# Kernel optimization log

Hardware: AMD Instinct MI355X
Metric: run time of the kernel (lower is better)

The kernel has to match this reference:

```python
import jax, jax.numpy as jnp
import numpy as np

B, T, D, H, E, TOP_K = 2, 2048, 1024, 4096, 8, 2


def setup_inputs() -> dict:
    key = jax.random.key(0)
    ks = jax.random.split(key, 7)
    s_d = 1.0 / np.sqrt(D)
    s_h = 1.0 / np.sqrt(H)
    return {
        "x": jax.random.normal(ks[0], (B, T, D), dtype=jnp.float32),
        "gate_w": jax.random.uniform(ks[1], (D, E), minval=-s_d, maxval=s_d, dtype=jnp.float32),
        "gate_b": jax.random.uniform(ks[2], (E,), minval=-s_d, maxval=s_d, dtype=jnp.float32),
        "w1": jax.random.uniform(ks[3], (E, D, H), minval=-s_d, maxval=s_d, dtype=jnp.float32),
        "b1": jax.random.uniform(ks[4], (E, H), minval=-s_d, maxval=s_d, dtype=jnp.float32),
        "w2": jax.random.uniform(ks[5], (E, H, D), minval=-s_h, maxval=s_h, dtype=jnp.float32),
        "b2": jax.random.uniform(ks[6], (E, D), minval=-s_h, maxval=s_h, dtype=jnp.float32),
    }


def reference(x, gate_w, gate_b, w1, b1, w2, b2):
    Bsz, Tn, Din = x.shape
    x_flat = x.reshape(-1, Din)                       # [N, D]
    N = x_flat.shape[0]
    gating_logits = x_flat @ gate_w + gate_b          # [N, E]
    weights, indices = jax.lax.top_k(gating_logits, TOP_K)
    weights = jax.nn.softmax(weights, axis=-1).astype(x.dtype)
    # scatter top-k weights into dense dispatch tensor [N, E]
    dispatch = jnp.zeros((N, E), dtype=x.dtype).at[jnp.arange(N)[:, None], indices].set(weights)
    # NOTE: faithful to original - gate weight multiplies the expert INPUT
    # and again the expert OUTPUT (double weighting through the GELU MLP).
    dispatched_x = dispatch[:, :, None] * x_flat[:, None, :]       # [N, E, D]
    h = jax.nn.gelu(jnp.einsum('ned,edh->neh', dispatched_x, w1) + b1, approximate=False)
    expert_out = jnp.einsum('neh,ehd->ned', h, w2) + b2            # [N, E, D]
    combined = jnp.sum(dispatch[:, :, None] * expert_out, axis=1)  # [N, D]
    final = combined.reshape(Bsz, Tn, -1)
    return final, gating_logits
```

## Files before the change

kernel.cpp:

```cpp
#include <hip/hip_runtime.h>
#include <hip/hip_bf16.h>
#include <math.h>

#define NTOK 4096
#define DDIM 1024
#define HDIM 4096
#define NEXP 8
#define CAP  4096
#define ROWCAP 9216
#define MAXTILES 72

typedef __attribute__((ext_vector_type(8))) short short8;
typedef __attribute__((ext_vector_type(4))) float f32x4;

#define GLOAD_LDS16(g, l) __builtin_amdgcn_global_load_lds( \
    (const __attribute__((address_space(1))) void*)(g),     \
    (__attribute__((address_space(3))) void*)(l), 16, 0, 0)

__global__ __launch_bounds__(256) void gating_kernel(
    const float* __restrict__ x, const float* __restrict__ gw,
    const float* __restrict__ gb, float* __restrict__ logits_out,
    int* __restrict__ counts, int* __restrict__ tok, float* __restrict__ gate,
    int* __restrict__ eA, int* __restrict__ sA, float* __restrict__ gA) {
  int t = blockIdx.x;
  int tid = threadIdx.x;
  float p[NEXP];
#pragma unroll
  for (int e = 0; e < NEXP; ++e) p[e] = 0.f;
  const float* xr = x + (size_t)t * DDIM;
  for (int d = tid; d < DDIM; d += 256) {
    float xv = xr[d];
    const float* wr = gw + (size_t)d * NEXP;
#pragma unroll
    for (int e = 0; e < NEXP; ++e) p[e] += xv * wr[e];
  }
#pragma unroll
  for (int off = 32; off > 0; off >>= 1)
#pragma unroll
    for (int e = 0; e < NEXP; ++e) p[e] += __shfl_xor(p[e], off, 64);
  __shared__ float red[4][NEXP];
  int wave = tid >> 6, lane = tid & 63;
  if (lane == 0)
#pragma unroll
    for (int e = 0; e < NEXP; ++e) red[wave][e] = p[e];
  __syncthreads();
  if (tid < NEXP) {
    float v = red[0][tid] + red[1][tid] + red[2][tid] + red[3][tid] + gb[tid];
    logits_out[(size_t)t * NEXP + tid] = v;
    red[0][tid] = v;
  }
  __syncthreads();
  if (tid == 0) {
    float v[NEXP];
#pragma unroll
    for (int e = 0; e < NEXP; ++e) v[e] = red[0][e];
    int i0 = 0;
#pragma unroll
    for (int e = 1; e < NEXP; ++e) if (v[e] > v[i0]) i0 = e;
    int i1 = (i0 == 0) ? 1 : 0;
#pragma unroll
    for (int e = 0; e < NEXP; ++e) if (e != i0 && v[e] > v[i1]) i1 = e;
    float e1 = expf(v[i1] - v[i0]);
    float s = 1.f + e1;
    float g0 = 1.f / s, g1 = e1 / s;
    int s0 = atomicAdd(&counts[i0], 1);
    tok[i0 * CAP + s0] = t; gate[i0 * CAP + s0] = g0;
    int s1 = atomicAdd(&counts[i1], 1);
    tok[i1 * CAP + s1] = t; gate[i1 * CAP + s1] = g1;
    eA[2 * t] = i0; sA[2 * t] = s0; gA[2 * t] = g0;
    eA[2 * t + 1] = i1; sA[2 * t + 1] = s1; gA[2 * t + 1] = g1;
  }
}

__global__ void sched_kernel(const int* __restrict__ counts, int* __restrict__ poff,
                             int* __restrict__ tileE, int* __restrict__ tileR,
                             int* __restrict__ nTiles) {
  if (threadIdx.x == 0) {
    int acc = 0, nt = 0;
    for (int e = 0; e < NEXP; ++e) {
      poff[e] = acc;
      int tl = (counts[e] + 127) >> 7;
      for (int t = 0; t < tl; ++t) { tileE[nt] = e; tileR[nt] = acc + t * 128; ++nt; }
      acc += tl << 7;
    }
    poff[NEXP] = acc;
    nTiles[0] = nt;
  }
}

__global__ __launch_bounds__(256) void transpose_kernel(
    const float* __restrict__ in, __hip_bfloat16* __restrict__ out, int R, int C) {
  __shared__ float tile[64 * 65];
  int e = blockIdx.z;
  int c0 = blockIdx.x * 64, r0 = blockIdx.y * 64;
  const float* inp = in + (size_t)e * R * C;
  __hip_bfloat16* outp = out + (size_t)e * R * C;
  int tx = threadIdx.x & 15, ty = threadIdx.x >> 4;
#pragma unroll
  for (int i = 0; i < 64; i += 16) {
    float4 v = *(const float4*)(inp + (size_t)(r0 + ty + i) * C + c0 + tx * 4);
    float* dst = tile + (ty + i) * 65 + tx * 4;
    dst[0] = v.x; dst[1] = v.y; dst[2] = v.z; dst[3] = v.w;
  }
  __syncthreads();
  int c = threadIdx.x >> 3;
  int rb = (threadIdx.x & 7) * 8;
#pragma unroll
  for (int p = 0; p < 2; ++p) {
    int cc = c + p * 32;
    union { unsigned short u[8]; short8 v8; } pk;
#pragma unroll
    for (int j = 0; j < 8; ++j) {
      __hip_bfloat16 h = __float2bfloat16(tile[(rb + j) * 65 + cc]);
      pk.u[j] = *(unsigned short*)&h;
    }
    *(short8*)(outp + (size_t)(c0 + cc) * R + r0 + rb) = pk.v8;
  }
}

__global__ __launch_bounds__(256) void gather_kernel(
    const float* __restrict__ x, const int* __restrict__ counts,
    const int* __restrict__ poff, const int* __restrict__ tok,
    const float* __restrict__ gate, __hip_bfloat16* __restrict__ Xg) {
  int e = blockIdx.y, r = blockIdx.x;
  int pc = poff[e + 1] - poff[e];
  if (r >= pc) return;
  int row = poff[e] + r;
  int tid = threadIdx.x;
  __hip_bfloat16* orow = Xg + (size_t)row * DDIM;
  if (r < counts[e]) {
    int t = tok[e * CAP + r];
    float g = gate[e * CAP + r];
    float4 v = ((const float4*)(x + (size_t)t * DDIM))[tid];
    union { unsigned short u[4]; uint2 q; } pk;
    __hip_bfloat16 h0 = __float2bfloat16(v.x * g);
    __hip_bfloat16 h1 = __float2bfloat16(v.y * g);
    __hip_bfloat16 h2 = __float2bfloat16(v.z * g);
    __hip_bfloat16 h3 = __float2bfloat16(v.w * g);
    pk.u[0] = *(unsigned short*)&h0; pk.u[1] = *(unsigned short*)&h1;
    pk.u[2] = *(unsigned short*)&h2; pk.u[3] = *(unsigned short*)&h3;
    ((uint2*)orow)[tid] = pk.q;
  } else {
    uint2 z; z.x = 0; z.y = 0;
    ((uint2*)orow)[tid] = z;
  }
}

template <int EPI>
__global__ __launch_bounds__(256) void moe_gemm(
    const __hip_bfloat16* __restrict__ A, const __hip_bfloat16* __restrict__ B,
    const float* __restrict__ bias, __hip_bfloat16* __restrict__ Hout,
    float* __restrict__ Pout, const int* __restrict__ tileE,
    const int* __restrict__ tileR, const int* __restrict__ nTiles,
    int K, int Nn) {
  int ty = blockIdx.y;
  if (ty >= nTiles[0]) return;
  int e = tileE[ty];
  int rowBase = tileR[ty];
  int colBase = blockIdx.x * 128;

  __shared__ __align__(16) char As[128 * 64];
  __shared__ __align__(16) char Bs[128 * 64];

  const char* Ae = (const char*)A + (size_t)rowBase * K * 2;
  const char* Be = (const char*)B + ((size_t)e * Nn + colBase) * (size_t)K * 2;

  int tid = threadIdx.x;
  int wave = tid >> 6, lane = tid & 63;
  int srow = lane >> 2;
  int cg = (((lane & 3) ^ ((lane >> 3) & 3)) << 4);

  f32x4 acc[4][4] = {};

  int wm = (wave >> 1) * 64, wn = (wave & 1) * 64;
  int frm = lane & 15;
  int fsw = (((lane >> 4) ^ ((lane >> 1) & 3)) << 4);

  int kPer = (EPI == 1) ? (K >> 1) : K;
  int kLo = blockIdx.z * kPer, kHi = kLo + kPer;

  for (int k0 = kLo; k0 < kHi; k0 += 32) {
    __syncthreads();
#pragma unroll
    for (int c = 0; c < 2; ++c) {
      int ch = wave * 2 + c;
      int r = ch * 16 + srow;
      GLOAD_LDS16(Ae + ((size_t)r * K + k0) * 2 + cg, As + ch * 1024 + lane * 16);
      GLOAD_LDS16(Be + ((size_t)r * K + k0) * 2 + cg, Bs + ch * 1024 + lane * 16);
    }
    __syncthreads();
    short8 af[4], bfr[4];
#pragma unroll
    for (int i = 0; i < 4; ++i) {
      af[i]  = *(const short8*)(As + (wm + i * 16 + frm) * 64 + fsw);
      bfr[i] = *(const short8*)(Bs + (wn + i * 16 + frm) * 64 + fsw);
    }
#pragma unroll
    for (int i = 0; i < 4; ++i)
#pragma unroll
      for (int j = 0; j < 4; ++j)
        acc[i][j] = __builtin_amdgcn_mfma_f32_16x16x32_bf16(af[i], bfr[j], acc[i][j], 0, 0, 0);
  }

  int cq = lane >> 4, cn = lane & 15;
  if (EPI == 0) {
#pragma unroll
    for (int i = 0; i < 4; ++i) {
#pragma unroll
      for (int j = 0; j < 4; ++j) {
        int col = colBase + wn + j * 16 + cn;
        float bv = bias[e * Nn + col];
#pragma unroll
        for (int r = 0; r < 4; ++r) {
          int row = rowBase + wm + i * 16 + cq * 4 + r;
          float v = acc[i][j][r] + bv;
          v = 0.5f * v * (1.0f + erff(v * 0.70710678118f));
          Hout[(size_t)row * Nn + col] = __float2bfloat16(v);
        }
      }
    }
  } else {
    float* Pp = Pout + ((size_t)blockIdx.z * ROWCAP + rowBase) * DDIM;
#pragma unroll
    for (int i = 0; i < 4; ++i) {
#pragma unroll
      for (int j = 0; j < 4; ++j) {
        int col = colBase + wn + j * 16 + cn;
#pragma unroll
        for (int r = 0; r < 4; ++r) {
          int row = wm + i * 16 + cq * 4 + r;
          Pp[(size_t)row * DDIM + col] = acc[i][j][r];
        }
      }
    }
  }
}

__global__ __launch_bounds__(256) void combine_kernel(
    const float* __restrict__ P, const float* __restrict__ b2,
    const int* __restrict__ poff, const int* __restrict__ eA,
    const int* __restrict__ sA, const float* __restrict__ gA,
    float* __restrict__ outF) {
  int t = blockIdx.x, c = threadIdx.x;
  int e0 = eA[2 * t], e1 = eA[2 * t + 1];
  int r0 = poff[e0] + sA[2 * t], r1 = poff[e1] + sA[2 * t + 1];
  float g0 = gA[2 * t], g1 = gA[2 * t + 1];
  float4 a0 = ((const float4*)(P + (size_t)r0 * DDIM))[c];
  float4 a1 = ((const float4*)(P + ((size_t)ROWCAP + r0) * DDIM))[c];
  float4 b0 = ((const float4*)(P + (size_t)r1 * DDIM))[c];
  float4 b1 = ((const float4*)(P + ((size_t)ROWCAP + r1) * DDIM))[c];
  float4 bb0 = ((const float4*)(b2 + (size_t)e0 * DDIM))[c];
  float4 bb1 = ((const float4*)(b2 + (size_t)e1 * DDIM))[c];
  float4 o;
  o.x = g0 * (a0.x + a1.x + bb0.x) + g1 * (b0.x + b1.x + bb1.x);
  o.y = g0 * (a0.y + a1.y + bb0.y) + g1 * (b0.y + b1.y + bb1.y);
  o.z = g0 * (a0.z + a1.z + bb0.z) + g1 * (b0.z + b1.z + bb1.z);
  o.w = g0 * (a0.w + a1.w + bb0.w) + g1 * (b0.w + b1.w + bb1.w);
  ((float4*)(outF + (size_t)t * DDIM))[c] = o;
}

extern "C" void kernel_launch(void* const* d_in, const int* in_sizes, int n_in,
                              void* d_out, int out_size, void* d_ws, size_t ws_size,
                              hipStream_t stream) {
  const float* x  = (const float*)d_in[0];
  const float* gw = (const float*)d_in[1];
  const float* gb = (const float*)d_in[2];
  const float* w1 = (const float*)d_in[3];
  const float* b1 = (const float*)d_in[4];
  const float* w2 = (const float*)d_in[5];
  const float* b2 = (const float*)d_in[6];

  float* outF = (float*)d_out;
  float* outL = outF + (size_t)NTOK * DDIM;

  size_t off = 0;
  char* base = (char*)d_ws;
  auto alloc = [&](size_t bytes) {
    void* r = base + off;
    off += (bytes + 255) & ~(size_t)255;
    return r;
  };
  __hip_bfloat16* wT1 = (__hip_bfloat16*)alloc((size_t)NEXP * HDIM * DDIM * 2);
  __hip_bfloat16* Xg  = (__hip_bfloat16*)alloc((size_t)ROWCAP * DDIM * 2);
  __hip_bfloat16* wT2 = (__hip_bfloat16*)alloc((size_t)NEXP * DDIM * HDIM * 2);
  __hip_bfloat16* Hact= (__hip_bfloat16*)alloc((size_t)ROWCAP * HDIM * 2);
  int*   tok    = (int*)alloc((size_t)NEXP * CAP * 4);
  float* gate   = (float*)alloc((size_t)NEXP * CAP * 4);
  int*   eA     = (int*)alloc((size_t)NTOK * 2 * 4);
  int*   sA     = (int*)alloc((size_t)NTOK * 2 * 4);
  float* gA     = (float*)alloc((size_t)NTOK * 2 * 4);
  int*   counts = (int*)alloc(64);
  int*   poff   = (int*)alloc(64);
  int*   tileE  = (int*)alloc(MAXTILES * 4);
  int*   tileR  = (int*)alloc(MAXTILES * 4);
  int*   nTiles = (int*)alloc(64);
  float* P      = (float*)wT1;

  hipMemsetAsync(counts, 0, 64, stream);
  gating_kernel<<<NTOK, 256, 0, stream>>>(x, gw, gb, outL, counts, tok, gate, eA, sA, gA);
  sched_kernel<<<1, 64, 0, stream>>>(counts, poff, tileE, tileR, nTiles);
  transpose_kernel<<<dim3(HDIM / 64, DDIM / 64, NEXP), 256, 0, stream>>>(w1, wT1, DDIM, HDIM);
  transpose_kernel<<<dim3(DDIM / 64, HDIM / 64, NEXP), 256, 0, stream>>>(w2, wT2, HDIM, DDIM);
  gather_kernel<<<dim3(CAP, NEXP), 256, 0, stream>>>(x, counts, poff, tok, gate, Xg);
  moe_gemm<0><<<dim3(HDIM / 128, MAXTILES, 1), 256, 0, stream>>>(
      Xg, wT1, b1, Hact, nullptr, tileE, tileR, nTiles, DDIM, HDIM);
  moe_gemm<1><<<dim3(DDIM / 128, MAXTILES, 2), 256, 0, stream>>>(
      Hact, wT2, b2, nullptr, P, tileE, tileR, nTiles, HDIM, DDIM);
  combine_kernel<<<NTOK, 256, 0, stream>>>(P, b2, poff, eA, sA, gA, outF);
}
```

Before: 720.4 us.

## Remap GEMM blocks per XCD, fuse weight transposes, use tanh GELU

Remaps the flat block index in both expert GEMMs so that blocks landing on the same XCD share column tiles of the weights, aiming at better L2 reuse. Merges the two weight transpose launches into a single kernel. Replaces the exact erf GELU with the tanh-style approximation computed through a sigmoid and fast exp, which trades exactness against the reference's exact GELU for cheaper math.

```diff
diff --git a/kernel.cpp b/kernel.cpp
--- a/kernel.cpp
+++ b/kernel.cpp
@@ -88,13 +88,25 @@
   }
 }
 
-__global__ __launch_bounds__(256) void transpose_kernel(
-    const float* __restrict__ in, __hip_bfloat16* __restrict__ out, int R, int C) {
+__global__ __launch_bounds__(256) void transpose_all(
+    const float* __restrict__ w1, const float* __restrict__ w2,
+    __hip_bfloat16* __restrict__ wT1, __hip_bfloat16* __restrict__ wT2) {
   __shared__ float tile[64 * 65];
-  int e = blockIdx.z;
-  int c0 = blockIdx.x * 64, r0 = blockIdx.y * 64;
-  const float* inp = in + (size_t)e * R * C;
-  __hip_bfloat16* outp = out + (size_t)e * R * C;
+  int id = blockIdx.x;
+  const float* inp; __hip_bfloat16* outp; int R, C, bx, by;
+  if (id < 8192) {
+    int e = id >> 10, rem = id & 1023;
+    bx = rem & 63; by = rem >> 6;
+    R = 1024; C = 4096;
+    inp = w1 + (size_t)e * R * C; outp = wT1 + (size_t)e * R * C;
+  } else {
+    id -= 8192;
+    int e = id >> 10, rem = id & 1023;
+    bx = rem & 15; by = rem >> 4;
+    R = 4096; C = 1024;
+    inp = w2 + (size_t)e * R * C; outp = wT2 + (size_t)e * R * C;
+  }
+  int c0 = bx * 64, r0 = by * 64;
   int tx = threadIdx.x & 15, ty = threadIdx.x >> 4;
 #pragma unroll
   for (int i = 0; i < 64; i += 16) {
@@ -153,11 +165,18 @@
     float* __restrict__ Pout, const int* __restrict__ tileE,
     const int* __restrict__ tileR, const int* __restrict__ nTiles,
     int K, int Nn) {
-  int ty = blockIdx.y;
+  int f = (blockIdx.z * gridDim.y + blockIdx.y) * gridDim.x + blockIdx.x;
+  int xcd = f & 7, seq = f >> 3;
+  int ct, ty, kz;
+  if (EPI == 0) {
+    ct = xcd * 4 + (seq & 3); ty = seq >> 2; kz = 0;
+  } else {
+    ct = xcd; ty = seq % MAXTILES; kz = seq / MAXTILES;
+  }
   if (ty >= nTiles[0]) return;
   int e = tileE[ty];
   int rowBase = tileR[ty];
-  int colBase = blockIdx.x * 128;
+  int colBase = ct * 128;
 
   __shared__ __align__(16) char As[128 * 64];
   __shared__ __align__(16) char Bs[128 * 64];
@@ -177,7 +196,7 @@
   int fsw = (((lane >> 4) ^ ((lane >> 1) & 3)) << 4);
 
   int kPer = (EPI == 1) ? (K >> 1) : K;
-  int kLo = blockIdx.z * kPer, kHi = kLo + kPer;
+  int kLo = kz * kPer, kHi = kLo + kPer;
 
   for (int k0 = kLo; k0 < kHi; k0 += 32) {
     __syncthreads();
@@ -214,13 +233,14 @@
         for (int r = 0; r < 4; ++r) {
           int row = rowBase + wm + i * 16 + cq * 4 + r;
           float v = acc[i][j][r] + bv;
-          v = 0.5f * v * (1.0f + erff(v * 0.70710678118f));
+          float z = 1.5957691f * v * (1.0f + 0.044715f * v * v);
+          v = v / (1.0f + __expf(-z));
           Hout[(size_t)row * Nn + col] = __float2bfloat16(v);
         }
       }
     }
   } else {
-    float* Pp = Pout + ((size_t)blockIdx.z * ROWCAP + rowBase) * DDIM;
+    float* Pp = Pout + ((size_t)kz * ROWCAP + rowBase) * DDIM;
 #pragma unroll
     for (int i = 0; i < 4; ++i) {
 #pragma unroll
@@ -299,8 +319,7 @@
   hipMemsetAsync(counts, 0, 64, stream);
   gating_kernel<<<NTOK, 256, 0, stream>>>(x, gw, gb, outL, counts, tok, gate, eA, sA, gA);
   sched_kernel<<<1, 64, 0, stream>>>(counts, poff, tileE, tileR, nTiles);
-  transpose_kernel<<<dim3(HDIM / 64, DDIM / 64, NEXP), 256, 0, stream>>>(w1, wT1, DDIM, HDIM);
-  transpose_kernel<<<dim3(DDIM / 64, HDIM / 64, NEXP), 256, 0, stream>>>(w2, wT2, HDIM, DDIM);
+  transpose_all<<<16384, 256, 0, stream>>>(w1, w2, wT1, wT2);
   gather_kernel<<<dim3(CAP, NEXP), 256, 0, stream>>>(x, counts, poff, tok, gate, Xg);
   moe_gemm<0><<<dim3(HDIM / 128, MAXTILES, 1), 256, 0, stream>>>(
       Xg, wT1, b1, Hact, nullptr, tileE, tileR, nTiles, DDIM, HDIM);
```

Measured after the change: 717.3 us. No clear change (-0.4%).
